# Kernel optimization log

Measured on AMD Instinct MI355X. Metric: run time of the kernel, lower is better.

## Reference

```python
import jax, jax.numpy as jnp
import numpy as np

NU_TAB, NM_TAB = 200000, 50000   # embedding table sizes
NU, NM = 100000, 20000           # nodes in batch
E = 300000                       # edges per direction
EMB, HID, OUT, H = 64, 64, 64, 4


def _ln(x, g, b):
    m = x.mean(-1, keepdims=True)
    v = ((x - m) ** 2).mean(-1, keepdims=True)
    return g * (x - m) * jax.lax.rsqrt(v + 1e-5) + b


def _act(x):
    return jax.nn.leaky_relu(x, 0.2)


def _gatv2(x_src, x_dst, ei, ea, Wl, bl, Wr, br, We, att, bias, concat):
    # GATv2Conv (PyG semantics): e_ij = leaky_relu(xl_j + xr_i + We*ea, 0.2);
    # alpha = segment_softmax(<att, e_ij>) over edges into i; out_i = sum alpha*xl_j
    n_dst = x_dst.shape[0]
    heads, C = att.shape
    xl = (x_src @ Wl + bl).reshape(-1, heads, C)   # [n_src, H, C]
    xr = (x_dst @ Wr + br).reshape(-1, heads, C)   # [n_dst, H, C]
    s, d = ei[0], ei[1]
    e = jax.nn.leaky_relu(xl[s] + xr[d] + (ea @ We).reshape(-1, heads, C), 0.2)  # [E,H,C]
    logit = (e * att).sum(-1)                       # [E, H]
    mx = jax.lax.stop_gradient(jax.ops.segment_max(logit, d, num_segments=n_dst))
    mx = jnp.where(jnp.isfinite(mx), mx, 0.0)
    ex = jnp.exp(logit - mx[d])
    den = jax.ops.segment_sum(ex, d, num_segments=n_dst)
    alpha = ex / (den[d] + 1e-16)                   # [E, H]
    out = jax.ops.segment_sum(xl[s] * alpha[..., None], d, num_segments=n_dst)  # [n_dst,H,C]
    out = out.reshape(n_dst, heads * C) if concat else out.mean(1)
    return out + bias


def setup_inputs() -> dict:
    key = jax.random.key(0)
    ks = iter(jax.random.split(key, 80))
    def nrm(shape, s=0.1):
        return jax.random.normal(next(ks), shape, jnp.float32) * s
    inp = {}
    inp['user_ids'] = jax.random.randint(next(ks), (NU,), 0, NU_TAB)
    inp['movie_ids'] = jax.random.randint(next(ks), (NM,), 0, NM_TAB)
    src_u = jax.random.randint(next(ks), (E,), 0, NU)
    dst_m = jax.random.randint(next(ks), (E,), 0, NM)
    inp['edge_index_um'] = jnp.stack([src_u, dst_m])           # user -> movie
    inp['edge_index_mu'] = jnp.stack([dst_m, src_u])           # movie -> user (reverse)
    ea = jax.random.uniform(next(ks), (E, 1), jnp.float32, 0.5, 5.0)
    inp['edge_attr_um'] = ea
    inp['edge_attr_mu'] = ea
    inp['user_emb'] = nrm((NU_TAB, EMB))
    inp['movie_emb'] = nrm((NM_TAB, EMB))
    inp['W_user'] = nrm((EMB, HID)); inp['b_user'] = jnp.zeros((HID,), jnp.float32)
    inp['W_movie'] = nrm((EMB, HID)); inp['b_movie'] = jnp.zeros((HID,), jnp.float32)
    def gat(prefix, in_dim, out_dim, concat):
        hc = H * out_dim
        inp[prefix + '_Wl'] = nrm((in_dim, hc))
        inp[prefix + '_bl'] = jnp.zeros((hc,), jnp.float32)
        inp[prefix + '_Wr'] = nrm((in_dim, hc))
        inp[prefix + '_br'] = jnp.zeros((hc,), jnp.float32)
        inp[prefix + '_We'] = nrm((1, hc))
        inp[prefix + '_att'] = nrm((H, out_dim))
        inp[prefix + '_b'] = jnp.zeros((hc if concat else out_dim,), jnp.float32)
    gat('l0um', HID, HID, True)
    gat('l0mu', HID, HID, True)
    gat('l1um', HID * H, OUT, False)
    gat('l1mu', HID * H, OUT, False)
    for name, dim in [('0u', HID * H), ('0m', HID * H), ('1u', OUT), ('1m', OUT)]:
        inp['g' + name] = jnp.ones((dim,), jnp.float32)
        inp['be' + name] = jnp.zeros((dim,), jnp.float32)
    return inp


def reference(user_ids, movie_ids, edge_index_um, edge_index_mu, edge_attr_um, edge_attr_mu,
              user_emb, movie_emb, W_user, b_user, W_movie, b_movie,
              l0um_Wl, l0um_bl, l0um_Wr, l0um_br, l0um_We, l0um_att, l0um_b,
              l0mu_Wl, l0mu_bl, l0mu_Wr, l0mu_br, l0mu_We, l0mu_att, l0mu_b,
              l1um_Wl, l1um_bl, l1um_Wr, l1um_br, l1um_We, l1um_att, l1um_b,
              l1mu_Wl, l1mu_bl, l1mu_Wr, l1mu_br, l1mu_We, l1mu_att, l1mu_b,
              g0u, be0u, g0m, be0m, g1u, be1u, g1m, be1m):
    xu = user_emb[user_ids] @ W_user + b_user      # [NU, HID]
    xm = movie_emb[movie_ids] @ W_movie + b_movie  # [NM, HID]
    # layer 0 (concat=True); HeteroConv sum is trivial: one incoming edge type per node type
    xm1 = _gatv2(xu, xm, edge_index_um, edge_attr_um, l0um_Wl, l0um_bl, l0um_Wr, l0um_br, l0um_We, l0um_att, l0um_b, True)
    xu1 = _gatv2(xm, xu, edge_index_mu, edge_attr_mu, l0mu_Wl, l0mu_bl, l0mu_Wr, l0mu_br, l0mu_We, l0mu_att, l0mu_b, True)
    xu1 = _act(_ln(xu1, g0u, be0u))
    xm1 = _act(_ln(xm1, g0m, be0m))
    # layer 1 (concat=False -> mean over heads)
    xm2 = _gatv2(xu1, xm1, edge_index_um, edge_attr_um, l1um_Wl, l1um_bl, l1um_Wr, l1um_br, l1um_We, l1um_att, l1um_b, False)
    xu2 = _gatv2(xm1, xu1, edge_index_mu, edge_attr_mu, l1mu_Wl, l1mu_bl, l1mu_Wr, l1mu_br, l1mu_We, l1mu_att, l1mu_b, False)
    xu2 = _act(_ln(xu2, g1u, be1u))
    xm2 = _act(_ln(xm2, g1m, be1m))
    return (xu2, xm2)
```

## Files before the change

kernel.cpp:

```cpp
#include <hip/hip_runtime.h>
#include <hip/hip_bf16.h>
#include <cstdint>

typedef __hip_bfloat16 bf16;
#define CDIV(a,b) (((a)+(b)-1)/(b))

typedef __attribute__((ext_vector_type(8))) short short8;
typedef __attribute__((ext_vector_type(8))) unsigned short usht8;
typedef __attribute__((ext_vector_type(4))) float f32x4v;

struct us4 { unsigned short x, y, z, w; };

__device__ __forceinline__ float lrelu02(float x) { return fmaxf(x, 0.f) + 0.2f * fminf(x, 0.f); }

__device__ __forceinline__ float b2f(unsigned short u) {
    return __uint_as_float((unsigned)u << 16);
}
__device__ __forceinline__ unsigned short f2b(float f) {
    unsigned u = __float_as_uint(f);
    unsigned r = u + 0x7FFFu + ((u >> 16) & 1u);
    return (unsigned short)(r >> 16);
}

__device__ __forceinline__ int swz(int row, int kg) {
    return row * 32 + (kg ^ ((row >> 1) & 3)) * 8;
}

__global__ void fill_i32(int* __restrict__ p, int v, long n) {
    long i = (long)blockIdx.x * blockDim.x + threadIdx.x;
    long st = (long)gridDim.x * blockDim.x;
    for (; i < n; i += st) p[i] = v;
}

__global__ void hist2_kernel(const int* __restrict__ edm, const int* __restrict__ edu,
                             int* __restrict__ deg_m, int* __restrict__ deg_u, int E) {
    int e = blockIdx.x * blockDim.x + threadIdx.x;
    if (e < E) atomicAdd(&deg_m[edm[e]], 1);
    else if (e < 2 * E) atomicAdd(&deg_u[edu[e - E]], 1);
}

#define SCAN_T 256
#define SCAN_E 16
__global__ void __launch_bounds__(SCAN_T) scan1_dual_kernel(
    const int* __restrict__ deg0, int* __restrict__ off0, int* __restrict__ bsum0, int n0,
    const int* __restrict__ deg1, int* __restrict__ off1, int* __restrict__ bsum1, int n1)
{
    const int* deg = blockIdx.y ? deg1 : deg0;
    int* off  = blockIdx.y ? off1 : off0;
    int* bsum = blockIdx.y ? bsum1 : bsum0;
    const int n = blockIdx.y ? n1 : n0;

    __shared__ int lds[SCAN_T];
    const int tb = blockIdx.x * (SCAN_T * SCAN_E) + threadIdx.x * SCAN_E;
    int v[SCAN_E];
    int tot = 0;
#pragma unroll
    for (int j = 0; j < SCAN_E; ++j) {
        v[j] = (tb + j < n) ? deg[tb + j] : 0;
        tot += v[j];
    }
    lds[threadIdx.x] = tot;
    __syncthreads();
    for (int s = 1; s < SCAN_T; s <<= 1) {
        int t = (threadIdx.x >= s) ? lds[threadIdx.x - s] : 0;
        __syncthreads();
        lds[threadIdx.x] += t;
        __syncthreads();
    }
    int run = (threadIdx.x > 0) ? lds[threadIdx.x - 1] : 0;
#pragma unroll
    for (int j = 0; j < SCAN_E; ++j) {
        if (tb + j < n) off[tb + j] = run;
        run += v[j];
    }
    if (threadIdx.x == SCAN_T - 1) bsum[blockIdx.x] = lds[SCAN_T - 1];
}
__global__ void scan2_dual_kernel(int* __restrict__ bm, int nbm, int* __restrict__ bu, int nbu) {
    int t = threadIdx.x & 63;
    int* b = (threadIdx.x >= 64) ? bu : bm;
    int nb = (threadIdx.x >= 64) ? nbu : nbm;
    int orig = (t < nb) ? b[t] : 0;
    int v = orig;
    for (int s = 1; s < 64; s <<= 1) {
        int u = __shfl_up(v, s);
        if (t >= s) v += u;
    }
    if (t < nb) b[t] = v - orig;
}
__global__ void scan3_dual_kernel(int* __restrict__ off0, const int* __restrict__ bsum0, int n0,
                                  int* __restrict__ off1, const int* __restrict__ bsum1, int n1) {
    int* off = blockIdx.y ? off1 : off0;
    const int* bsum = blockIdx.y ? bsum1 : bsum0;
    const int n = blockIdx.y ? n1 : n0;
    int i = blockIdx.x * blockDim.x + threadIdx.x;
    if (i < n) off[i] += bsum[i / (SCAN_T * SCAN_E)];
}

__global__ void csr_fill2_kernel(
    const int* __restrict__ esm, const int* __restrict__ edm, const float* __restrict__ eam,
    const int* __restrict__ offm, int* __restrict__ curm, int2* __restrict__ recm,
    const int* __restrict__ esu, const int* __restrict__ edu, const float* __restrict__ eau,
    const int* __restrict__ offu, int* __restrict__ curu, int2* __restrict__ recu, int E)
{
    int e = blockIdx.x * blockDim.x + threadIdx.x;
    if (e < E) {
        int d = edm[e];
        int r = atomicAdd(&curm[d], 1);
        int2 q; q.x = esm[e]; q.y = __float_as_int(eam[e]);
        recm[offm[d] + r] = q;
    } else if (e < 2 * E) {
        e -= E;
        int d = edu[e];
        int r = atomicAdd(&curu[d], 1);
        int2 q; q.x = esu[e]; q.y = __float_as_int(eau[e]);
        recu[offu[d] + r] = q;
    }
}

struct TxArgs {
    const float* src[4];
    unsigned short* dst[4];
};
__global__ void txp_kernel(TxArgs a) {
    const int m = blockIdx.y;
    const int K = 256, N = 256;
    const long total = (long)K * N;
    const float* __restrict__ s = a.src[m];
    unsigned short* __restrict__ d = a.dst[m];
    for (long i = (long)blockIdx.x * blockDim.x + threadIdx.x; i < total;
         i += (long)gridDim.x * blockDim.x) {
        int k = (int)(i >> 8), nn = (int)(i & 255);
        d[(long)nn * K + k] = f2b(s[i]);
    }
}

__global__ void cw_kernel(const float* __restrict__ Wu, const float* __restrict__ bu,
                          const float* __restrict__ Wa, const float* __restrict__ ba,
                          const float* __restrict__ Wb, const float* __restrict__ bb,
                          unsigned short* __restrict__ wt, float* __restrict__ bc)
{
    int tid = blockIdx.x * blockDim.x + threadIdx.x;
    if (tid < 512 * 64) {
        int nn = tid >> 6, k = tid & 63;
        const float* Ws = (nn < 256) ? Wa : Wb;
        int nc = nn & 255;
        float s = 0.f;
        for (int c = 0; c < 64; ++c) s = fmaf(Wu[k * 64 + c], Ws[c * 256 + nc], s);
        wt[nn * 64 + k] = f2b(s);
    } else if (tid < 512 * 64 + 512) {
        int nn = tid - 512 * 64;
        const float* Ws = (nn < 256) ? Wa : Wb;
        const float* bs = (nn < 256) ? ba : bb;
        int nc = nn & 255;
        float s = bs[nc];
        for (int c = 0; c < 64; ++c) s = fmaf(bu[c], Ws[c * 256 + nc], s);
        bc[nn] = s;
    }
}

template<int K, bool GATHER>
__global__ void __launch_bounds__(256) gemm256_kernel(
    const void* __restrict__ Asrc, const int* __restrict__ ids,
    const unsigned short* __restrict__ Wt0, const unsigned short* __restrict__ Wt1,
    const float* __restrict__ bias0, const float* __restrict__ bias1,
    unsigned short* __restrict__ Y0, unsigned short* __restrict__ Y1, int n)
{
    const int t = threadIdx.x;
    const int wid = t >> 6, lane = t & 63;
    const int half = blockIdx.x & 1;
    const int row0 = (blockIdx.x >> 1) * 64;
    const unsigned short* __restrict__ Wt = half ? Wt1 : Wt0;
    const float* __restrict__ bias = half ? bias1 : bias0;
    unsigned short* __restrict__ Y = half ? Y1 : Y0;

    __shared__ unsigned short SMEM[64 * 32 + 256 * 32];
    unsigned short* As = SMEM;
    unsigned short* Ws = SMEM + 64 * 32;

    f32x4v acc[4][4];
#pragma unroll
    for (int rt = 0; rt < 4; ++rt)
#pragma unroll
        for (int ct = 0; ct < 4; ++ct) acc[rt][ct] = (f32x4v){0.f, 0.f, 0.f, 0.f};

    const int r_st = t >> 2, kg_st = t & 3;
    const int grow = row0 + r_st;
    long abase = 0;
    if (grow < n) abase = GATHER ? (long)ids[grow] * K : (long)grow * K;

    for (int kt = 0; kt < K / 32; ++kt) {
        usht8 av = (usht8)0;
        if (grow < n) {
            if (GATHER) {
                const float* p = (const float*)Asrc + abase + kt * 32 + kg_st * 8;
#pragma unroll
                for (int j = 0; j < 8; ++j) av[j] = f2b(p[j]);
            } else {
                av = *(const usht8*)((const unsigned short*)Asrc + abase + kt * 32 + kg_st * 8);
            }
        }
        *(usht8*)&As[swz(r_st, kg_st)] = av;
#pragma unroll
        for (int i = 0; i < 4; ++i) {
            int idx = t + i * 256;
            int c = idx >> 2, kg = idx & 3;
            *(usht8*)&Ws[swz(c, kg)] = *(const usht8*)&Wt[(long)c * K + kt * 32 + kg * 8];
        }
        __syncthreads();

        const int kgrp = lane >> 4;
        short8 af[4];
#pragma unroll
        for (int rt = 0; rt < 4; ++rt)
            af[rt] = *(const short8*)&As[swz(rt * 16 + (lane & 15), kgrp)];
#pragma unroll
        for (int ct = 0; ct < 4; ++ct) {
            int col = wid * 64 + ct * 16 + (lane & 15);
            short8 bfr = *(const short8*)&Ws[swz(col, kgrp)];
#pragma unroll
            for (int rt = 0; rt < 4; ++rt)
                acc[rt][ct] = __builtin_amdgcn_mfma_f32_16x16x32_bf16(af[rt], bfr, acc[rt][ct], 0, 0, 0);
        }
        __syncthreads();
    }

    float bb[4];
#pragma unroll
    for (int ct = 0; ct < 4; ++ct) bb[ct] = bias[wid * 64 + ct * 16 + (lane & 15)];

#pragma unroll
    for (int rh = 0; rh < 2; ++rh) {
#pragma unroll
        for (int rt = rh * 2; rt < rh * 2 + 2; ++rt) {
#pragma unroll
            for (int ct = 0; ct < 4; ++ct) {
                int col = wid * 64 + ct * 16 + (lane & 15);
#pragma unroll
                for (int j = 0; j < 4; ++j) {
                    int rl = rt * 16 + (lane >> 4) * 4 + j - rh * 32;
                    SMEM[rl * 256 + col] = f2b(acc[rt][ct][j] + bb[ct]);
                }
            }
        }
        __syncthreads();
#pragma unroll
        for (int i = 0; i < 4; ++i) {
            int idx = t + i * 256;
            int rl = idx >> 5, cseg = (idx & 31) * 8;
            int row = row0 + rh * 32 + rl;
            if (row < n)
                *(usht8*)&Y[(long)row * 256 + cseg] = *(const usht8*)&SMEM[rl * 256 + cseg];
        }
        __syncthreads();
    }
}

template<bool CONCAT>
__global__ void __launch_bounds__(256) gat_fused_kernel(
    const int* __restrict__ deg, const int* __restrict__ off,
    const int2* __restrict__ rec,
    const bf16* __restrict__ xl, const bf16* __restrict__ xr,
    const float* __restrict__ We, const float* __restrict__ att,
    const float* __restrict__ bias,
    const float* __restrict__ g, const float* __restrict__ be,
    void* __restrict__ yout, int n)
{
    const int lane = threadIdx.x & 63;
    const int d = blockIdx.x * 4 + (threadIdx.x >> 6);
    if (d >= n) return;
    const int q = lane & 15;
    const int c0 = ((lane >> 4) << 6) + (q << 2);

    float4 We4 = *(const float4*)(We + c0);
    float4 att4 = *(const float4*)(att + c0);
    us4 xrv = *(const us4*)((const unsigned short*)xr + (long)d * 256 + c0);
    float xr4[4] = {b2f(xrv.x), b2f(xrv.y), b2f(xrv.z), b2f(xrv.w)};

    float m = -1e30f, den = 0.f;
    float acc[4] = {0.f, 0.f, 0.f, 0.f};

    const int dg = deg[d], o0 = off[d];
    const unsigned short* __restrict__ xlp = (const unsigned short*)xl;

    for (int base = 0; base < dg; base += 64) {
        int2 r;
        if (base + lane < dg) r = rec[o0 + base + lane];
        else { r.x = 0; r.y = 0; }
        const int cnt = min(dg - base, 64);
        for (int j = 0; j < cnt; j += 4) {
            int sA[4], aB[4];
            us4 xvA[4];
#pragma unroll
            for (int u = 0; u < 4; ++u) {
                sA[u] = __builtin_amdgcn_readlane(r.x, j + u);
                aB[u] = __builtin_amdgcn_readlane(r.y, j + u);
            }
#pragma unroll
            for (int u = 0; u < 4; ++u)
                xvA[u] = *(const us4*)(xlp + (long)sA[u] * 256 + c0);
#pragma unroll
            for (int u = 0; u < 4; ++u) {
                const float a = __int_as_float(aB[u]);
                float xv[4] = {b2f(xvA[u].x), b2f(xvA[u].y), b2f(xvA[u].z), b2f(xvA[u].w)};
                float part = 0.f;
#pragma unroll
                for (int i = 0; i < 4; ++i) {
                    float t = xv[i] + fmaf(a, (&We4.x)[i], xr4[i]);
                    part = fmaf(lrelu02(t), (&att4.x)[i], part);
                }
#pragma unroll
                for (int st = 1; st < 16; st <<= 1) part += __shfl_xor(part, st);
                float l = (j + u < cnt) ? part : -1e30f;
                float mn = fmaxf(m, l);
                float sc = __expf(m - mn);
                float p  = __expf(l - mn);
                m = mn;
                den = fmaf(den, sc, p);
#pragma unroll
                for (int i = 0; i < 4; ++i) acc[i] = fmaf(acc[i], sc, p * xv[i]);
            }
        }
    }

    const float id = 1.f / (den + 1e-16f);
    if (CONCAT) {
        float4 bi = *(const float4*)(bias + c0);
        float v[4], s1 = 0.f, s2 = 0.f;
#pragma unroll
        for (int i = 0; i < 4; ++i) {
            v[i] = fmaf(acc[i], id, (&bi.x)[i]);
            s1 += v[i]; s2 = fmaf(v[i], v[i], s2);
        }
#pragma unroll
        for (int st = 1; st < 64; st <<= 1) {
            s1 += __shfl_xor(s1, st);
            s2 += __shfl_xor(s2, st);
        }
        float mean = s1 * (1.f / 256.f);
        float var = s2 * (1.f / 256.f) - mean * mean;
        float rr = rsqrtf(var + 1e-5f);
        float4 gg = *(const float4*)(g + c0);
        float4 bb = *(const float4*)(be + c0);
        us4 o;
        o.x = f2b(lrelu02(fmaf((&gg.x)[0] * rr, v[0] - mean, (&bb.x)[0])));
        o.y = f2b(lrelu02(fmaf((&gg.x)[1] * rr, v[1] - mean, (&bb.x)[1])));
        o.z = f2b(lrelu02(fmaf((&gg.x)[2] * rr, v[2] - mean, (&bb.x)[2])));
        o.w = f2b(lrelu02(fmaf((&gg.x)[3] * rr, v[3] - mean, (&bb.x)[3])));
        *(us4*)((unsigned short*)yout + (long)d * 256 + c0) = o;
    } else {
        float vh[4];
#pragma unroll
        for (int i = 0; i < 4; ++i) vh[i] = acc[i] * id;
#pragma unroll
        for (int st = 16; st < 64; st <<= 1)
#pragma unroll
            for (int i = 0; i < 4; ++i) vh[i] += __shfl_xor(vh[i], st);
        const int oc = q << 2;
        float4 bi = *(const float4*)(bias + oc);
        float v[4], s1 = 0.f, s2 = 0.f;
#pragma unroll
        for (int i = 0; i < 4; ++i) {
            v[i] = fmaf(0.25f, vh[i], (&bi.x)[i]);
            s1 += v[i]; s2 = fmaf(v[i], v[i], s2);
        }
#pragma unroll
        for (int st = 1; st < 16; st <<= 1) {
            s1 += __shfl_xor(s1, st);
            s2 += __shfl_xor(s2, st);
        }
        float mean = s1 * (1.f / 64.f);
        float var = s2 * (1.f / 64.f) - mean * mean;
        float rr = rsqrtf(var + 1e-5f);
        float4 gg = *(const float4*)(g + oc);
        float4 bb = *(const float4*)(be + oc);
        if (lane < 16) {
            float4 o;
            o.x = lrelu02(fmaf((&gg.x)[0] * rr, v[0] - mean, (&bb.x)[0]));
            o.y = lrelu02(fmaf((&gg.x)[1] * rr, v[1] - mean, (&bb.x)[1]));
            o.z = lrelu02(fmaf((&gg.x)[2] * rr, v[2] - mean, (&bb.x)[2]));
            o.w = lrelu02(fmaf((&gg.x)[3] * rr, v[3] - mean, (&bb.x)[3]));
            *(float4*)((float*)yout + (long)d * 64 + oc) = o;
        }
    }
}

extern "C" void kernel_launch(void* const* d_in, const int* in_sizes, int n_in,
                              void* d_out, int out_size, void* d_ws, size_t ws_size,
                              hipStream_t stream)
{
    auto F = [&](int i) { return (const float*)d_in[i]; };
    auto I = [&](int i) { return (const int*)d_in[i]; };

    const int NU = in_sizes[0];
    const int NM = in_sizes[1];
    const int E  = in_sizes[2] / 2;

    const int* user_ids  = I(0);
    const int* movie_ids = I(1);
    const int* ei_um = I(2);
    const int* ei_mu = I(3);
    const float* ea_um = F(4);
    const float* ea_mu = F(5);
    const float* user_emb  = F(6);
    const float* movie_emb = F(7);
    const float* W_user = F(8),  *b_user = F(9);
    const float* W_movie = F(10), *b_movie = F(11);
    const int L0UM = 12, L0MU = 19, L1UM = 26, L1MU = 33;
    const float* g0u = F(40), *be0u = F(41);
    const float* g0m = F(42), *be0m = F(43);
    const float* g1u = F(44), *be1u = F(45);
    const float* g1m = F(46), *be1m = F(47);

    char* w = (char*)d_ws;
    size_t off = 0;
    auto alloc = [&](size_t bytes) -> void* {
        void* p = w + off;
        off = (off + bytes + 255) & ~(size_t)255;
        return p;
    };
    bf16* UB1 = (bf16*)alloc((size_t)NU * 256 * 2);
    bf16* UB2 = (bf16*)alloc((size_t)NU * 256 * 2);
    bf16* UB3 = (bf16*)alloc((size_t)NU * 256 * 2);
    bf16* MB1 = (bf16*)alloc((size_t)NM * 256 * 2);
    bf16* MB2 = (bf16*)alloc((size_t)NM * 256 * 2);
    bf16* MB3 = (bf16*)alloc((size_t)NM * 256 * 2);
    int* degcur = (int*)alloc((size_t)2 * (NM + NU) * 4);
    int* deg_m = degcur;
    int* deg_u = degcur + NM;
    int* cur_m = degcur + NM + NU;
    int* cur_u = degcur + 2 * NM + NU;
    int* off_m = (int*)alloc((size_t)NM * 4);
    int* off_u = (int*)alloc((size_t)NU * 4);
    int2* rec_m = (int2*)alloc((size_t)(E + 4) * 8);
    int2* rec_u = (int2*)alloc((size_t)(E + 4) * 8);
    int* bsum_m = (int*)alloc(64 * 4);
    int* bsum_u = (int*)alloc(64 * 4);
    unsigned short* wt_l1um_l = (unsigned short*)alloc(256 * 256 * 2);
    unsigned short* wt_l1mu_r = (unsigned short*)alloc(256 * 256 * 2);
    unsigned short* wt_l1um_r = (unsigned short*)alloc(256 * 256 * 2);
    unsigned short* wt_l1mu_l = (unsigned short*)alloc(256 * 256 * 2);
    unsigned short* wt_c_user  = (unsigned short*)alloc(512 * 64 * 2);
    unsigned short* wt_c_movie = (unsigned short*)alloc(512 * 64 * 2);
    float* bc_user  = (float*)alloc(512 * 4);
    float* bc_movie = (float*)alloc(512 * 4);
    if (off > ws_size) return;

    float* out_u = (float*)d_out;
    float* out_m = out_u + (size_t)NU * 64;

    const int FB = 256;

    TxArgs tx;
    tx.src[0] = F(L1UM+0); tx.dst[0] = wt_l1um_l;
    tx.src[1] = F(L1MU+2); tx.dst[1] = wt_l1mu_r;
    tx.src[2] = F(L1UM+2); tx.dst[2] = wt_l1um_r;
    tx.src[3] = F(L1MU+0); tx.dst[3] = wt_l1mu_l;
    txp_kernel<<<dim3(64, 4), 256, 0, stream>>>(tx);
    cw_kernel<<<CDIV(512 * 64 + 512, 256), 256, 0, stream>>>(
        W_user, b_user, F(L0UM+0), F(L0UM+1), F(L0MU+2), F(L0MU+3), wt_c_user, bc_user);
    cw_kernel<<<CDIV(512 * 64 + 512, 256), 256, 0, stream>>>(
        W_movie, b_movie, F(L0UM+2), F(L0UM+3), F(L0MU+0), F(L0MU+1), wt_c_movie, bc_movie);

    fill_i32<<<CDIV(2 * (NM + NU), FB), FB, 0, stream>>>(degcur, 0, (long)2 * (NM + NU));
    hist2_kernel<<<CDIV(2 * E, FB), FB, 0, stream>>>(ei_um + E, ei_mu + E, deg_m, deg_u, E);
    const int nbm = CDIV(NM, SCAN_T * SCAN_E), nbu = CDIV(NU, SCAN_T * SCAN_E);
    scan1_dual_kernel<<<dim3(max(nbm, nbu), 2), SCAN_T, 0, stream>>>(
        deg_m, off_m, bsum_m, NM, deg_u, off_u, bsum_u, NU);
    scan2_dual_kernel<<<1, 128, 0, stream>>>(bsum_m, nbm, bsum_u, nbu);
    scan3_dual_kernel<<<dim3(CDIV(max(NM, NU), FB), 2), FB, 0, stream>>>(
        off_m, bsum_m, NM, off_u, bsum_u, NU);
    csr_fill2_kernel<<<CDIV(2 * E, FB), FB, 0, stream>>>(
        ei_um, ei_um + E, ea_um, off_m, cur_m, rec_m,
        ei_mu, ei_mu + E, ea_mu, off_u, cur_u, rec_u, E);

    gemm256_kernel<64, true><<<CDIV(NU, 64) * 2, 256, 0, stream>>>(
        user_emb, user_ids, wt_c_user, wt_c_user + 256 * 64, bc_user, bc_user + 256,
        (unsigned short*)UB1, (unsigned short*)UB2, NU);
    gemm256_kernel<64, true><<<CDIV(NM, 64) * 2, 256, 0, stream>>>(
        movie_emb, movie_ids, wt_c_movie, wt_c_movie + 256 * 64, bc_movie, bc_movie + 256,
        (unsigned short*)MB1, (unsigned short*)MB3, NM);

    gat_fused_kernel<true><<<CDIV(NM, 4), 256, 0, stream>>>(
        deg_m, off_m, rec_m, UB1, MB1, F(L0UM+4), F(L0UM+5), F(L0UM+6), g0m, be0m, MB2, NM);
    gat_fused_kernel<true><<<CDIV(NU, 4), 256, 0, stream>>>(
        deg_u, off_u, rec_u, MB3, UB2, F(L0MU+4), F(L0MU+5), F(L0MU+6), g0u, be0u, UB1, NU);

    gemm256_kernel<256, false><<<CDIV(NU, 64) * 2, 256, 0, stream>>>(
        (unsigned short*)UB1, nullptr, wt_l1um_l, wt_l1mu_r, F(L1UM+1), F(L1MU+3),
        (unsigned short*)UB2, (unsigned short*)UB3, NU);
    gemm256_kernel<256, false><<<CDIV(NM, 64) * 2, 256, 0, stream>>>(
        (unsigned short*)MB2, nullptr, wt_l1um_r, wt_l1mu_l, F(L1UM+3), F(L1MU+1),
        (unsigned short*)MB1, (unsigned short*)MB3, NM);

    gat_fused_kernel<false><<<CDIV(NM, 4), 256, 0, stream>>>(
        deg_m, off_m, rec_m, UB2, MB1, F(L1UM+4), F(L1UM+5), F(L1UM+6), g1m, be1m, out_m, NM);
    gat_fused_kernel<false><<<CDIV(NU, 4), 256, 0, stream>>>(
        deg_u, off_u, rec_u, MB3, UB3, F(L1MU+4), F(L1MU+5), F(L1MU+6), g1u, be1u, out_u, NU);
}
```

Baseline: 417.0 us.

## Persistent-grid GAT kernel with lazy softmax rescale and abs-based leaky ReLU

Turns the fused GAT aggregation into a grid-stride persistent kernel capped at 2048 blocks, so per-wave constants (We, att, bias, LN params) are loaded once and reused across many destination nodes. The online softmax now handles 4 edges per step and only rescales the accumulator when the group max exceeds the running max by more than 8. This cuts per-edge exp and rescale work. Leaky ReLU dot with att is rewritten as 0.6*t + 0.4*|t| with premultiplied weights. The delayed rescale lets exponents grow up to e^8 before renormalising, which is safe for fp32 but changes rounding slightly.

```diff
diff --git a/kernel.cpp b/kernel.cpp
--- a/kernel.cpp
+++ b/kernel.cpp
@@ -266,120 +266,137 @@
     void* __restrict__ yout, int n)
 {
     const int lane = threadIdx.x & 63;
-    const int d = blockIdx.x * 4 + (threadIdx.x >> 6);
-    if (d >= n) return;
     const int q = lane & 15;
     const int c0 = ((lane >> 4) << 6) + (q << 2);
+    const int wid0 = blockIdx.x * 4 + (threadIdx.x >> 6);
+    const int wstride = gridDim.x * 4;
 
     float4 We4 = *(const float4*)(We + c0);
     float4 att4 = *(const float4*)(att + c0);
-    us4 xrv = *(const us4*)((const unsigned short*)xr + (long)d * 256 + c0);
-    float xr4[4] = {b2f(xrv.x), b2f(xrv.y), b2f(xrv.z), b2f(xrv.w)};
-
-    float m = -1e30f, den = 0.f;
-    float acc[4] = {0.f, 0.f, 0.f, 0.f};
-
-    const int dg = deg[d], o0 = off[d];
+    float att06[4], att04[4];
+#pragma unroll
+    for (int i = 0; i < 4; ++i) {
+        att06[i] = 0.6f * (&att4.x)[i];
+        att04[i] = 0.4f * (&att4.x)[i];
+    }
+    const int ec = CONCAT ? c0 : (q << 2);
+    float4 bi = *(const float4*)(bias + ec);
+    float4 gg = *(const float4*)(g + ec);
+    float4 bb = *(const float4*)(be + ec);
+
     const unsigned short* __restrict__ xlp = (const unsigned short*)xl;
 
-    for (int base = 0; base < dg; base += 64) {
-        int2 r;
-        if (base + lane < dg) r = rec[o0 + base + lane];
-        else { r.x = 0; r.y = 0; }
-        const int cnt = min(dg - base, 64);
-        for (int j = 0; j < cnt; j += 4) {
-            int sA[4], aB[4];
-            us4 xvA[4];
-#pragma unroll
-            for (int u = 0; u < 4; ++u) {
-                sA[u] = __builtin_amdgcn_readlane(r.x, j + u);
-                aB[u] = __builtin_amdgcn_readlane(r.y, j + u);
-            }
-#pragma unroll
-            for (int u = 0; u < 4; ++u)
-                xvA[u] = *(const us4*)(xlp + (long)sA[u] * 256 + c0);
-#pragma unroll
-            for (int u = 0; u < 4; ++u) {
-                const float a = __int_as_float(aB[u]);
-                float xv[4] = {b2f(xvA[u].x), b2f(xvA[u].y), b2f(xvA[u].z), b2f(xvA[u].w)};
-                float part = 0.f;
-#pragma unroll
-                for (int i = 0; i < 4; ++i) {
-                    float t = xv[i] + fmaf(a, (&We4.x)[i], xr4[i]);
-                    part = fmaf(lrelu02(t), (&att4.x)[i], part);
+    for (int d = wid0; d < n; d += wstride) {
+        us4 xrv = *(const us4*)((const unsigned short*)xr + (long)d * 256 + c0);
+        float xr4[4] = {b2f(xrv.x), b2f(xrv.y), b2f(xrv.z), b2f(xrv.w)};
+
+        float m = -1e30f, den = 0.f;
+        float acc[4] = {0.f, 0.f, 0.f, 0.f};
+
+        const int dg = deg[d], o0 = off[d];
+
+        for (int base = 0; base < dg; base += 64) {
+            int2 r;
+            if (base + lane < dg) r = rec[o0 + base + lane];
+            else { r.x = 0; r.y = 0; }
+            const int cnt = min(dg - base, 64);
+            for (int j = 0; j < cnt; j += 4) {
+                us4 xvA[4];
+                int aB[4];
+#pragma unroll
+                for (int u = 0; u < 4; ++u) {
+                    int s = __builtin_amdgcn_readlane(r.x, j + u);
+                    aB[u] = __builtin_amdgcn_readlane(r.y, j + u);
+                    xvA[u] = *(const us4*)(xlp + (long)s * 256 + c0);
                 }
-#pragma unroll
-                for (int st = 1; st < 16; st <<= 1) part += __shfl_xor(part, st);
-                float l = (j + u < cnt) ? part : -1e30f;
-                float mn = fmaxf(m, l);
-                float sc = __expf(m - mn);
-                float p  = __expf(l - mn);
-                m = mn;
-                den = fmaf(den, sc, p);
-#pragma unroll
-                for (int i = 0; i < 4; ++i) acc[i] = fmaf(acc[i], sc, p * xv[i]);
-            }
-        }
-    }
-
-    const float id = 1.f / (den + 1e-16f);
-    if (CONCAT) {
-        float4 bi = *(const float4*)(bias + c0);
-        float v[4], s1 = 0.f, s2 = 0.f;
-#pragma unroll
-        for (int i = 0; i < 4; ++i) {
-            v[i] = fmaf(acc[i], id, (&bi.x)[i]);
-            s1 += v[i]; s2 = fmaf(v[i], v[i], s2);
-        }
-#pragma unroll
-        for (int st = 1; st < 64; st <<= 1) {
-            s1 += __shfl_xor(s1, st);
-            s2 += __shfl_xor(s2, st);
-        }
-        float mean = s1 * (1.f / 256.f);
-        float var = s2 * (1.f / 256.f) - mean * mean;
-        float rr = rsqrtf(var + 1e-5f);
-        float4 gg = *(const float4*)(g + c0);
-        float4 bb = *(const float4*)(be + c0);
-        us4 o;
-        o.x = f2b(lrelu02(fmaf((&gg.x)[0] * rr, v[0] - mean, (&bb.x)[0])));
-        o.y = f2b(lrelu02(fmaf((&gg.x)[1] * rr, v[1] - mean, (&bb.x)[1])));
-        o.z = f2b(lrelu02(fmaf((&gg.x)[2] * rr, v[2] - mean, (&bb.x)[2])));
-        o.w = f2b(lrelu02(fmaf((&gg.x)[3] * rr, v[3] - mean, (&bb.x)[3])));
-        *(us4*)((unsigned short*)yout + (long)d * 256 + c0) = o;
-    } else {
-        float vh[4];
-#pragma unroll
-        for (int i = 0; i < 4; ++i) vh[i] = acc[i] * id;
-#pragma unroll
-        for (int st = 16; st < 64; st <<= 1)
-#pragma unroll
-            for (int i = 0; i < 4; ++i) vh[i] += __shfl_xor(vh[i], st);
-        const int oc = q << 2;
-        float4 bi = *(const float4*)(bias + oc);
-        float v[4], s1 = 0.f, s2 = 0.f;
-#pragma unroll
-        for (int i = 0; i < 4; ++i) {
-            v[i] = fmaf(0.25f, vh[i], (&bi.x)[i]);
-            s1 += v[i]; s2 = fmaf(v[i], v[i], s2);
-        }
-#pragma unroll
-        for (int st = 1; st < 16; st <<= 1) {
-            s1 += __shfl_xor(s1, st);
-            s2 += __shfl_xor(s2, st);
-        }
-        float mean = s1 * (1.f / 64.f);
-        float var = s2 * (1.f / 64.f) - mean * mean;
-        float rr = rsqrtf(var + 1e-5f);
-        float4 gg = *(const float4*)(g + oc);
-        float4 bb = *(const float4*)(be + oc);
-        if (lane < 16) {
-            float4 o;
-            o.x = lrelu02(fmaf((&gg.x)[0] * rr, v[0] - mean, (&bb.x)[0]));
-            o.y = lrelu02(fmaf((&gg.x)[1] * rr, v[1] - mean, (&bb.x)[1]));
-            o.z = lrelu02(fmaf((&gg.x)[2] * rr, v[2] - mean, (&bb.x)[2]));
-            o.w = lrelu02(fmaf((&gg.x)[3] * rr, v[3] - mean, (&bb.x)[3]));
-            *(float4*)((float*)yout + (long)d * 64 + oc) = o;
+                float l[4], xvf[4][4];
+#pragma unroll
+                for (int u = 0; u < 4; ++u) {
+                    xvf[u][0] = b2f(xvA[u].x); xvf[u][1] = b2f(xvA[u].y);
+                    xvf[u][2] = b2f(xvA[u].z); xvf[u][3] = b2f(xvA[u].w);
+                    const float a = __int_as_float(aB[u]);
+                    float part = 0.f;
+#pragma unroll
+                    for (int i = 0; i < 4; ++i) {
+                        float t = xvf[u][i] + fmaf(a, (&We4.x)[i], xr4[i]);
+                        part = fmaf(att06[i], t, part);
+                        part = fmaf(att04[i], fabsf(t), part);
+                    }
+#pragma unroll
+                    for (int st = 1; st < 16; st <<= 1) part += __shfl_xor(part, st);
+                    l[u] = (j + u < cnt) ? part : -1e30f;
+                }
+                float bmax = fmaxf(fmaxf(l[0], l[1]), fmaxf(l[2], l[3]));
+                if (__any(bmax > m + 8.f)) {
+                    float mn = fmaxf(m, bmax);
+                    float sc = __expf(m - mn);
+                    den *= sc;
+#pragma unroll
+                    for (int i = 0; i < 4; ++i) acc[i] *= sc;
+                    m = mn;
+                }
+#pragma unroll
+                for (int u = 0; u < 4; ++u) {
+                    float p = __expf(l[u] - m);
+                    den += p;
+#pragma unroll
+                    for (int i = 0; i < 4; ++i) acc[i] = fmaf(p, xvf[u][i], acc[i]);
+                }
+            }
+        }
+
+        const float id = 1.f / (den + 1e-16f);
+        if (CONCAT) {
+            float v[4], s1 = 0.f, s2 = 0.f;
+#pragma unroll
+            for (int i = 0; i < 4; ++i) {
+                v[i] = fmaf(acc[i], id, (&bi.x)[i]);
+                s1 += v[i]; s2 = fmaf(v[i], v[i], s2);
+            }
+#pragma unroll
+            for (int st = 1; st < 64; st <<= 1) {
+                s1 += __shfl_xor(s1, st);
+                s2 += __shfl_xor(s2, st);
+            }
+            float mean = s1 * (1.f / 256.f);
+            float var = s2 * (1.f / 256.f) - mean * mean;
+            float rr = rsqrtf(var + 1e-5f);
+            us4 o;
+            o.x = f2b(lrelu02(fmaf((&gg.x)[0] * rr, v[0] - mean, (&bb.x)[0])));
+            o.y = f2b(lrelu02(fmaf((&gg.x)[1] * rr, v[1] - mean, (&bb.x)[1])));
+            o.z = f2b(lrelu02(fmaf((&gg.x)[2] * rr, v[2] - mean, (&bb.x)[2])));
+            o.w = f2b(lrelu02(fmaf((&gg.x)[3] * rr, v[3] - mean, (&bb.x)[3])));
+            *(us4*)((unsigned short*)yout + (long)d * 256 + c0) = o;
+        } else {
+            float vh[4];
+#pragma unroll
+            for (int i = 0; i < 4; ++i) vh[i] = acc[i] * id;
+#pragma unroll
+            for (int st = 16; st < 64; st <<= 1)
+#pragma unroll
+                for (int i = 0; i < 4; ++i) vh[i] += __shfl_xor(vh[i], st);
+            float v[4], s1 = 0.f, s2 = 0.f;
+#pragma unroll
+            for (int i = 0; i < 4; ++i) {
+                v[i] = fmaf(0.25f, vh[i], (&bi.x)[i]);
+                s1 += v[i]; s2 = fmaf(v[i], v[i], s2);
+            }
+#pragma unroll
+            for (int st = 1; st < 16; st <<= 1) {
+                s1 += __shfl_xor(s1, st);
+                s2 += __shfl_xor(s2, st);
+            }
+            float mean = s1 * (1.f / 64.f);
+            float var = s2 * (1.f / 64.f) - mean * mean;
+            float rr = rsqrtf(var + 1e-5f);
+            if (lane < 16) {
+                float4 o;
+                o.x = lrelu02(fmaf((&gg.x)[0] * rr, v[0] - mean, (&bb.x)[0]));
+                o.y = lrelu02(fmaf((&gg.x)[1] * rr, v[1] - mean, (&bb.x)[1]));
+                o.z = lrelu02(fmaf((&gg.x)[2] * rr, v[2] - mean, (&bb.x)[2]));
+                o.w = lrelu02(fmaf((&gg.x)[3] * rr, v[3] - mean, (&bb.x)[3]));
+                *(float4*)((float*)yout + (long)d * 64 + (q << 2)) = o;
+            }
         }
     }
 }
@@ -480,9 +497,11 @@
         movie_emb, movie_ids, wt_c_movie, wt_c_movie + 256 * 64, bc_movie, bc_movie + 256,
         (unsigned short*)MB1, (unsigned short*)MB3, NM);
 
-    gat_fused_kernel<true><<<CDIV(NM, 4), 256, 0, stream>>>(
+    auto ggrid = [&](int n) { int b = CDIV(n, 4); if (b > 2048) b = 2048; return dim3((unsigned)b); };
+
+    gat_fused_kernel<true><<<ggrid(NM), 256, 0, stream>>>(
         deg_m, off_m, rec_m, UB1, MB1, F(L0UM+4), F(L0UM+5), F(L0UM+6), g0m, be0m, MB2, NM);
-    gat_fused_kernel<true><<<CDIV(NU, 4), 256, 0, stream>>>(
+    gat_fused_kernel<true><<<ggrid(NU), 256, 0, stream>>>(
         deg_u, off_u, rec_u, MB3, UB2, F(L0MU+4), F(L0MU+5), F(L0MU+6), g0u, be0u, UB1, NU);
 
     gemm256_kernel<256, false><<<CDIV(NU, 64) * 2, 256, 0, stream>>>(
@@ -492,8 +511,8 @@
         (unsigned short*)MB2, nullptr, wt_l1um_r, wt_l1mu_l, F(L1UM+3), F(L1MU+1),
         (unsigned short*)MB1, (unsigned short*)MB3, NM);
 
-    gat_fused_kernel<false><<<CDIV(NM, 4), 256, 0, stream>>>(
+    gat_fused_kernel<false><<<ggrid(NM), 256, 0, stream>>>(
         deg_m, off_m, rec_m, UB2, MB1, F(L1UM+4), F(L1UM+5), F(L1UM+6), g1m, be1m, out_m, NM);
-    gat_fused_kernel<false><<<CDIV(NU, 4), 256, 0, stream>>>(
+    gat_fused_kernel<false><<<ggrid(NU), 256, 0, stream>>>(
         deg_u, off_u, rec_u, MB3, UB3, F(L1MU+4), F(L1MU+5), F(L1MU+6), g1u, be1u, out_u, NU);
 }
```

After: 416.8 us. Within noise of the previous version (-0.1%).
